# Performance work log

Hardware: AMD Instinct MI355X
Metric: run time of the kernel (lower is better)

The kernel has to match this reference:

```python
import jax, jax.numpy as jnp
import numpy as np

IMG_H, IMG_W = 1024, 1024   # input_image_size used for box scaling
RH, RW = 40, 40             # hardcoded interpolate size
NUM_CLASSES = 599           # hardcoded class count


def setup_inputs() -> dict:
    key = jax.random.key(0)
    k1, k2, k3, k4 = jax.random.split(key, 4)
    B, C, H, W, N = 16, 256, 100, 100, 100
    features = jax.random.normal(k1, (B, C, H, W), dtype=jnp.float32)
    xy = jax.random.uniform(k2, (B, N, 2), minval=0.0, maxval=900.0)
    wh = jax.random.uniform(k3, (B, N, 2), minval=20.0, maxval=120.0)
    boxes = jnp.concatenate([xy, jnp.minimum(xy + wh, 1024.0)], axis=-1).astype(jnp.float32)
    gt_classes = jax.random.randint(k4, (B, N), 0, NUM_CLASSES).astype(jnp.int32)
    return {"features": features, "boxes": boxes, "gt_classes": gt_classes}


def reference(features, boxes, gt_classes):
    # features: [B,C,H,W] last-layer feature map; boxes: [B,N,4] xyxy in image coords
    B, C, H, W = features.shape
    # F.interpolate(..., mode='bilinear', align_corners=False) == half-pixel linear resize, no antialias
    resized = jax.image.resize(features, (B, C, RH, RW), method='bilinear', antialias=False)

    scale = jnp.array([RW / IMG_W, RH / IMG_H, RW / IMG_W, RH / IMG_H], dtype=boxes.dtype)
    b = jnp.round(boxes * scale).astype(jnp.int32)  # torch.round is also half-to-even
    x1 = jnp.maximum(b[..., 0], 0)
    y1 = jnp.maximum(b[..., 1], 0)
    x2 = jnp.minimum(b[..., 2], RW)
    y2 = jnp.minimum(b[..., 3], RH)
    valid = (x1 < x2) & (y1 < y2)
    # safe indices for the integral image (invalid boxes masked out later)
    x1s = jnp.clip(x1, 0, RW); x2s = jnp.clip(x2, 0, RW)
    y1s = jnp.clip(y1, 0, RH); y2s = jnp.clip(y2, 0, RH)

    # integral image -> exact box-average pooling (== adaptive_avg_pool2d to (1,1))
    ii = jnp.pad(resized, ((0, 0), (0, 0), (1, 0), (1, 0))).cumsum(axis=2).cumsum(axis=3)  # [B,C,RH+1,RW+1]

    def per_image(ii_i, x1, y1, x2, y2, v, cls):
        # ii_i: [C,RH+1,RW+1]; index arrays: [N]
        s = ii_i[:, y2, x2] - ii_i[:, y1, x2] - ii_i[:, y2, x1] + ii_i[:, y1, x1]  # [C,N]
        area = jnp.where(v, ((y2 - y1) * (x2 - x1)).astype(s.dtype), 1.0)
        pooled = (s / area).T * v[:, None].astype(s.dtype)  # [N,C], zeros for invalid boxes
        sums = jax.ops.segment_sum(pooled, cls, num_segments=NUM_CLASSES)           # [599,C]
        counts = jax.ops.segment_sum(v.astype(s.dtype), cls, num_segments=NUM_CLASSES)  # [599]
        # scatter-mean; classes with no valid boxes -> zeros (eval mode of the module)
        return jnp.where(counts[:, None] > 0, sums / jnp.maximum(counts, 1.0)[:, None], 0.0)

    return jax.vmap(per_image)(ii, x1s, y1s, x2s, y2s, valid, gt_classes)  # [B,599,C]
```

## Files before the change

### kernel.cpp

```cpp
#include <hip/hip_runtime.h>

#define BB 16
#define CC 256
#define HH 100
#define WW 100
#define NN 100
#define RH 40
#define RW 40
#define KK 599
#define KT 19
#define CT 8

__global__ __launch_bounds__(256) void pool_kernel(
    const float* __restrict__ feat, const float* __restrict__ boxes,
    const int* __restrict__ cls, float* __restrict__ dst, int ws_mode)
{
    __shared__ float tile[RH][RW + 1];
    __shared__ float sums[KK];
    __shared__ float cnts[KK];

    const int blk = blockIdx.x;
    const int b = blk >> 8;
    const int c = blk & 255;
    const int tid = threadIdx.x;

    const float* __restrict__ src = feat + (size_t)(b * CC + c) * (HH * WW);

    for (int idx = tid; idx < RH * RW; idx += 256) {
        int oy = idx / RW;
        int ox = idx - oy * RW;
        int iy0 = (5 * oy + 1) >> 1;
        int ix0 = (5 * ox + 1) >> 1;
        float fy = (oy & 1) ? 0.25f : 0.75f;
        float fx = (ox & 1) ? 0.25f : 0.75f;
        const float* r0 = src + iy0 * WW + ix0;
        float v00 = r0[0], v01 = r0[1];
        float v10 = r0[WW], v11 = r0[WW + 1];
        float top = (1.0f - fx) * v00 + fx * v01;
        float bot = (1.0f - fx) * v10 + fx * v11;
        tile[oy][ox] = (1.0f - fy) * top + fy * bot;
    }

    for (int k = tid; k < KK; k += 256) {
        sums[k] = 0.0f;
        cnts[k] = 0.0f;
    }
    __syncthreads();

    if (tid < NN) {
        const float* bp = boxes + (size_t)(b * NN + tid) * 4;
        const float sc = 0.0390625f;
        int x1 = (int)rintf(bp[0] * sc);
        int y1 = (int)rintf(bp[1] * sc);
        int x2 = (int)rintf(bp[2] * sc);
        int y2 = (int)rintf(bp[3] * sc);
        x1 = max(x1, 0); y1 = max(y1, 0);
        x2 = min(x2, RW); y2 = min(y2, RH);
        if (x1 < x2 && y1 < y2) {
            float s = 0.0f;
            for (int y = y1; y < y2; ++y)
                for (int x = x1; x < x2; ++x)
                    s += tile[y][x];
            float area = (float)((y2 - y1) * (x2 - x1));
            int k = cls[b * NN + tid];
            atomicAdd(&sums[k], s / area);
            atomicAdd(&cnts[k], 1.0f);
        }
    }
    __syncthreads();

    if (ws_mode) {
        float* o = dst + (size_t)(b * CC + c) * KK;
        for (int k = tid; k < KK; k += 256) {
            float cn = cnts[k];
            o[k] = (cn > 0.0f) ? (sums[k] / cn) : 0.0f;
        }
    } else {
        for (int k = tid; k < KK; k += 256) {
            float cn = cnts[k];
            dst[(size_t)(b * KK + k) * CC + c] = (cn > 0.0f) ? (sums[k] / cn) : 0.0f;
        }
    }
}

__global__ __launch_bounds__(256) void transpose_kernel(
    const float* __restrict__ ws, float* __restrict__ out)
{
    __shared__ float t[32][33];
    int blk = blockIdx.x;
    int b = blk / (KT * CT);
    int r = blk - b * (KT * CT);
    int kt = r / CT;
    int ct = r - kt * CT;
    int k0 = kt * 32;
    int c0 = ct * 32;
    int tx = threadIdx.x & 31;
    int ty = threadIdx.x >> 5;

    int k = k0 + tx;
    if (k < KK) {
        #pragma unroll
        for (int i = 0; i < 4; ++i) {
            int cl = ty + i * 8;
            t[cl][tx] = ws[(size_t)(b * CC + c0 + cl) * KK + k];
        }
    }
    __syncthreads();
    #pragma unroll
    for (int i = 0; i < 4; ++i) {
        int kl = ty + i * 8;
        int kk = k0 + kl;
        if (kk < KK)
            out[(size_t)(b * KK + kk) * CC + c0 + tx] = t[tx][kl];
    }
}

extern "C" void kernel_launch(void* const* d_in, const int* in_sizes, int n_in,
                              void* d_out, int out_size, void* d_ws, size_t ws_size,
                              hipStream_t stream) {
    const float* feat  = (const float*)d_in[0];
    const float* boxes = (const float*)d_in[1];
    const int*   cls   = (const int*)d_in[2];
    float* out = (float*)d_out;

    const size_t ws_need = (size_t)BB * CC * KK * sizeof(float);
    if (ws_size >= ws_need) {
        float* ws = (float*)d_ws;
        pool_kernel<<<BB * CC, 256, 0, stream>>>(feat, boxes, cls, ws, 1);
        transpose_kernel<<<BB * KT * CT, 256, 0, stream>>>(ws, out);
    } else {
        pool_kernel<<<BB * CC, 256, 0, stream>>>(feat, boxes, cls, out, 0);
    }
}
```

Measured before the change: 238.8 us.

## Replace workspace transpose with zero-fill plus sparse direct strided writes

The workspace write and separate transpose kernel are dropped. Output is now zero-filled by a vectorized float4 kernel, and the pool kernel writes only classes that have boxes straight into the [B,K,C] layout. Block indices are remapped so that consecutive blocks land on different images/channels, and box coordinates and class ids are loaded before the resize work. This avoids a full round trip through the workspace, at the cost of strided scattered stores and an extra launch.

```diff
diff --git a/kernel.cpp b/kernel.cpp
--- a/kernel.cpp
+++ b/kernel.cpp
@@ -8,21 +8,35 @@
 #define RH 40
 #define RW 40
 #define KK 599
-#define KT 19
-#define CT 8
+
+#define ZERO_BLOCKS 2396
+
+__global__ __launch_bounds__(256) void zero_kernel(float4* __restrict__ out)
+{
+    out[(size_t)blockIdx.x * 256 + threadIdx.x] = make_float4(0.f, 0.f, 0.f, 0.f);
+}
 
 __global__ __launch_bounds__(256) void pool_kernel(
     const float* __restrict__ feat, const float* __restrict__ boxes,
-    const int* __restrict__ cls, float* __restrict__ dst, int ws_mode)
+    const int* __restrict__ cls, float* __restrict__ out)
 {
     __shared__ float tile[RH][RW + 1];
     __shared__ float sums[KK];
     __shared__ float cnts[KK];
 
-    const int blk = blockIdx.x;
-    const int b = blk >> 8;
-    const int c = blk & 255;
+    const int raw = blockIdx.x;
+    const int L = (raw & 7) * (BB * CC / 8) + (raw >> 3);
+    const int b = L >> 8;
+    const int c = L & 255;
     const int tid = threadIdx.x;
+
+    float bx0 = 0.f, bx1 = 0.f, bx2 = 0.f, bx3 = 0.f;
+    int myk = 0;
+    if (tid < NN) {
+        const float* bp = boxes + (size_t)(b * NN + tid) * 4;
+        bx0 = bp[0]; bx1 = bp[1]; bx2 = bp[2]; bx3 = bp[3];
+        myk = cls[b * NN + tid];
+    }
 
     const float* __restrict__ src = feat + (size_t)(b * CC + c) * (HH * WW);
 
@@ -48,12 +62,11 @@
     __syncthreads();
 
     if (tid < NN) {
-        const float* bp = boxes + (size_t)(b * NN + tid) * 4;
         const float sc = 0.0390625f;
-        int x1 = (int)rintf(bp[0] * sc);
-        int y1 = (int)rintf(bp[1] * sc);
-        int x2 = (int)rintf(bp[2] * sc);
-        int y2 = (int)rintf(bp[3] * sc);
+        int x1 = (int)rintf(bx0 * sc);
+        int y1 = (int)rintf(bx1 * sc);
+        int x2 = (int)rintf(bx2 * sc);
+        int y2 = (int)rintf(bx3 * sc);
         x1 = max(x1, 0); y1 = max(y1, 0);
         x2 = min(x2, RW); y2 = min(y2, RH);
         if (x1 < x2 && y1 < y2) {
@@ -62,73 +75,28 @@
                 for (int x = x1; x < x2; ++x)
                     s += tile[y][x];
             float area = (float)((y2 - y1) * (x2 - x1));
-            int k = cls[b * NN + tid];
-            atomicAdd(&sums[k], s / area);
-            atomicAdd(&cnts[k], 1.0f);
+            atomicAdd(&sums[myk], s / area);
+            atomicAdd(&cnts[myk], 1.0f);
         }
     }
     __syncthreads();
 
-    if (ws_mode) {
-        float* o = dst + (size_t)(b * CC + c) * KK;
-        for (int k = tid; k < KK; k += 256) {
-            float cn = cnts[k];
-            o[k] = (cn > 0.0f) ? (sums[k] / cn) : 0.0f;
-        }
-    } else {
-        for (int k = tid; k < KK; k += 256) {
-            float cn = cnts[k];
-            dst[(size_t)(b * KK + k) * CC + c] = (cn > 0.0f) ? (sums[k] / cn) : 0.0f;
-        }
-    }
-}
-
-__global__ __launch_bounds__(256) void transpose_kernel(
-    const float* __restrict__ ws, float* __restrict__ out)
-{
-    __shared__ float t[32][33];
-    int blk = blockIdx.x;
-    int b = blk / (KT * CT);
-    int r = blk - b * (KT * CT);
-    int kt = r / CT;
-    int ct = r - kt * CT;
-    int k0 = kt * 32;
-    int c0 = ct * 32;
-    int tx = threadIdx.x & 31;
-    int ty = threadIdx.x >> 5;
-
-    int k = k0 + tx;
-    if (k < KK) {
-        #pragma unroll
-        for (int i = 0; i < 4; ++i) {
-            int cl = ty + i * 8;
-            t[cl][tx] = ws[(size_t)(b * CC + c0 + cl) * KK + k];
-        }
-    }
-    __syncthreads();
-    #pragma unroll
-    for (int i = 0; i < 4; ++i) {
-        int kl = ty + i * 8;
-        int kk = k0 + kl;
-        if (kk < KK)
-            out[(size_t)(b * KK + kk) * CC + c0 + tx] = t[tx][kl];
+    float* o = out + (size_t)b * KK * CC + c;
+    for (int k = tid; k < KK; k += 256) {
+        float cn = cnts[k];
+        if (cn > 0.0f) o[(size_t)k * CC] = sums[k] / cn;
     }
 }
 
 extern "C" void kernel_launch(void* const* d_in, const int* in_sizes, int n_in,
                               void* d_out, int out_size, void* d_ws, size_t ws_size,
                               hipStream_t stream) {
+    (void)d_ws; (void)ws_size; (void)in_sizes; (void)n_in; (void)out_size;
     const float* feat  = (const float*)d_in[0];
     const float* boxes = (const float*)d_in[1];
     const int*   cls   = (const int*)d_in[2];
     float* out = (float*)d_out;
 
-    const size_t ws_need = (size_t)BB * CC * KK * sizeof(float);
-    if (ws_size >= ws_need) {
-        float* ws = (float*)d_ws;
-        pool_kernel<<<BB * CC, 256, 0, stream>>>(feat, boxes, cls, ws, 1);
-        transpose_kernel<<<BB * KT * CT, 256, 0, stream>>>(ws, out);
-    } else {
-        pool_kernel<<<BB * CC, 256, 0, stream>>>(feat, boxes, cls, out, 0);
-    }
+    zero_kernel<<<ZERO_BLOCKS, 256, 0, stream>>>((float4*)out);
+    pool_kernel<<<BB * CC, 256, 0, stream>>>(feat, boxes, cls, out);
 }
```

After: 234.4 us. About the same (-1.8%).
